# Kernel tuning notes

Hardware: AMD Instinct MI355X
Metric: run time of the kernel (lower is better)

## Reference

```python
import jax, jax.numpy as jnp
import numpy as np

N = 100000


def gcn_conv(x, W, b, src, dst, deg_inv_sqrt, n):
    # PyG GCNConv: h = D^{-1/2} (A + I) D^{-1/2} (x W) + b
    h = x @ W  # [N, out]
    norm = deg_inv_sqrt[src] * deg_inv_sqrt[dst]  # [E+N]
    msgs = h[src] * norm[:, None]  # gathered + scaled messages
    out = jax.ops.segment_sum(msgs, dst, num_segments=n)
    return out + b


def _self_loops_and_norm(edge_index, n):
    src, dst = edge_index[0], edge_index[1]
    loop = jnp.arange(n, dtype=edge_index.dtype)
    src = jnp.concatenate([src, loop])
    dst = jnp.concatenate([dst, loop])
    deg = jax.ops.segment_sum(jnp.ones_like(dst, dtype=jnp.float32), dst, num_segments=n)
    deg_inv_sqrt = jnp.where(deg > 0, jax.lax.rsqrt(jnp.maximum(deg, 1.0)), 0.0)
    return src, dst, deg_inv_sqrt


def setup_inputs() -> dict:
    key = jax.random.key(0)
    k1, k2, k3, k4 = jax.random.split(key, 4)
    nfeat, nhid, nclass = 512, 256, 40
    E = 3200000
    x = jax.random.normal(k1, (N, nfeat), dtype=jnp.float32)
    edge_index = jax.random.randint(k2, (2, E), 0, N, dtype=jnp.int64)
    # Glorot-style init for GCNConv weights, zero bias (PyG default)
    W1 = jax.random.normal(k3, (nfeat, nhid), dtype=jnp.float32) / np.sqrt(nfeat)
    b1 = jnp.zeros((nhid,), dtype=jnp.float32)
    W2 = jax.random.normal(k4, (nhid, nclass), dtype=jnp.float32) / np.sqrt(nhid)
    b2 = jnp.zeros((nclass,), dtype=jnp.float32)
    return {"x": x, "W1": W1, "b1": b1, "W2": W2, "b2": b2, "edge_index": edge_index}


def reference(x, W1, b1, W2, b2, edge_index):
    src, dst, dis = _self_loops_and_norm(edge_index, N)
    h = gcn_conv(x, W1, b1, src, dst, dis, N)
    h = jax.nn.relu(h)
    # dropout(p=0.5) is identity in eval mode
    h = gcn_conv(h, W2, b2, src, dst, dis, N)
    return jax.nn.log_softmax(h, axis=1)
```

## Files before the change

kernel.cpp:

```cpp
#include <hip/hip_runtime.h>
#include <math.h>

#define NFEAT 512
#define NHID  256
#define NCLASS 40
#define NBUCK 782
#define BCAP  5120

typedef __attribute__((ext_vector_type(8))) short short8;
typedef __attribute__((ext_vector_type(4))) float f32x4;


__device__ __forceinline__ float bflo(unsigned u) {
    union { unsigned i; float f; } x; x.i = u << 16; return x.f;
}
__device__ __forceinline__ float bfhi(unsigned u) {
    union { unsigned i; float f; } x; x.i = u & 0xffff0000u; return x.f;
}
__device__ __forceinline__ unsigned short f2bf(float f) {
    union { float f; unsigned i; } x; x.f = f;
    unsigned r = x.i + 0x7fffu + ((x.i >> 16) & 1u);
    return (unsigned short)(r >> 16);
}
__device__ __forceinline__ unsigned pack2(float a, float b) {
    return (unsigned)f2bf(a) | ((unsigned)f2bf(b) << 16);
}


__global__ __launch_bounds__(256) void partcast_k(const float* __restrict__ W1,
                                                  unsigned short* __restrict__ WT,
                                                  const int* __restrict__ ei,
                                                  int* bucketCnt,
                                                  unsigned* __restrict__ binned, int E) {
    __shared__ int hist[NBUCK];
    __shared__ int sbase[NBUCK];
    __shared__ int lofs[NBUCK];
    int bid = blockIdx.x;
    int t = threadIdx.x;
    if (bid < (NFEAT * NHID) / 256) {
        int idx = bid * 256 + t;
        int k = idx >> 8;
        int nn = idx & 255;
        WT[(size_t)nn * NFEAT + k] = f2bf(W1[idx]);
        return;
    }
    int pb = bid - (NFEAT * NHID) / 256;
    for (int b = t; b < NBUCK; b += 256) { hist[b] = 0; lofs[b] = 0; }
    __syncthreads();
    int chunk = (E + 255) / 256;
    int beg = pb * chunk;
    int end = beg + chunk; if (end > E) end = E;
    for (int e = beg + t; e < end; e += 256) {
        int d = __builtin_nontemporal_load(ei + (size_t)E + e);
        atomicAdd(&hist[d >> 7], 1);
    }
    __syncthreads();
    for (int b = t; b < NBUCK; b += 256) {
        int h = hist[b];
        if (h) sbase[b] = atomicAdd(&bucketCnt[b], h);
    }
    __syncthreads();
    for (int e = beg + t; e < end; e += 256) {
        int s = __builtin_nontemporal_load(ei + e);
        int d = __builtin_nontemporal_load(ei + (size_t)E + e);
        int b = d >> 7;
        int off = sbase[b] + atomicAdd(&lofs[b], 1);
        __builtin_nontemporal_store(((unsigned)s << 7) | (unsigned)(d & 127),
                                    binned + (size_t)b * BCAP + off);
    }
}


__global__ __launch_bounds__(1024) void bscan_k(const int* __restrict__ bucketCnt,
                                                int* __restrict__ bbase,
                                                int* __restrict__ offs, int n, int E) {
    __shared__ int sd[1024];
    int t = threadIdx.x;
    int v = (t < NBUCK) ? bucketCnt[t] : 0;
    sd[t] = v;
    __syncthreads();
    for (int off = 1; off < 1024; off <<= 1) {
        int add = (t >= off) ? sd[t - off] : 0;
        __syncthreads();
        sd[t] += add;
        __syncthreads();
    }
    if (t < NBUCK) bbase[t] = sd[t] - v;
    if (t == 0) offs[n] = E;
}


__global__ __launch_bounds__(512) void fill2_k(const unsigned* __restrict__ binned,
                                               const int* __restrict__ bucketCnt,
                                               const int* __restrict__ bbase,
                                               int* __restrict__ offs,
                                               float* __restrict__ dis,
                                               int* __restrict__ csrs, int n) {
    __shared__ int h128[128];
    __shared__ int sd[128];
    __shared__ int lcur[128];
    int b = blockIdx.x;
    int t = threadIdx.x;
    int node0 = b << 7;
    int cbt = bucketCnt[b];
    size_t base_in = (size_t)b * BCAP;
    int gbase = bbase[b];
    if (t < 128) h128[t] = 0;
    __syncthreads();
    for (int e = t; e < cbt; e += 512) {
        unsigned u = binned[base_in + e];
        atomicAdd(&h128[u & 127], 1);
    }
    __syncthreads();
    int v = (t < 128) ? h128[t] : 0;
    if (t < 128) sd[t] = v;
    __syncthreads();
    for (int off = 1; off < 128; off <<= 1) {
        int add = (t < 128 && t >= off) ? sd[t - off] : 0;
        __syncthreads();
        if (t < 128) sd[t] += add;
        __syncthreads();
    }
    if (t < 128) {
        int excl = sd[t] - v;
        int nd = node0 + t;
        if (nd < n) {
            offs[nd] = gbase + excl;
            dis[nd] = rsqrtf((float)v + 1.0f);
        }
        lcur[t] = gbase + excl;
    }
    __syncthreads();
    for (int e = t; e < cbt; e += 512) {
        unsigned u = binned[base_in + e];
        int pos = atomicAdd(&lcur[u & 127], 1);
        csrs[pos] = (int)(u >> 7);
    }
}


__global__ __launch_bounds__(256) void gemm1_k(const float* __restrict__ X,
                                               const unsigned short* __restrict__ WT,
                                               const float* __restrict__ dis,
                                               unsigned short* __restrict__ H, int M) {
    __shared__ unsigned short as[64][72];
    __shared__ unsigned short bs[256][72];
    int t = threadIdx.x;
    int lane = t & 63;
    int w = t >> 6;
    int m0 = blockIdx.x * 64;
    int quad = lane >> 4;
    int r16 = lane & 15;

    f32x4 acc[4][4];
#pragma unroll
    for (int a = 0; a < 4; ++a)
#pragma unroll
        for (int b = 0; b < 4; ++b) acc[a][b] = (f32x4){0.f, 0.f, 0.f, 0.f};

    for (int k0 = 0; k0 < NFEAT; k0 += 64) {
        {
            int m = t >> 2;
            int c = (t & 3) * 16;
            int gi = m0 + m;
            float4 v0, v1, v2, v3;
            if (gi < M) {
                const float4* p = (const float4*)(X + (size_t)gi * NFEAT + k0 + c);
                v0 = p[0]; v1 = p[1]; v2 = p[2]; v3 = p[3];
            } else {
                v0 = v1 = v2 = v3 = make_float4(0.f, 0.f, 0.f, 0.f);
            }
            uint4 p0, p1;
            p0.x = pack2(v0.x, v0.y); p0.y = pack2(v0.z, v0.w);
            p0.z = pack2(v1.x, v1.y); p0.w = pack2(v1.z, v1.w);
            p1.x = pack2(v2.x, v2.y); p1.y = pack2(v2.z, v2.w);
            p1.z = pack2(v3.x, v3.y); p1.w = pack2(v3.z, v3.w);
            *(uint4*)&as[m][c] = p0;
            *(uint4*)&as[m][c + 8] = p1;
        }
        {
            const uint4* p = (const uint4*)(WT + (size_t)t * NFEAT + k0);
#pragma unroll
            for (int c = 0; c < 8; ++c) {
                uint4 q = p[c];
                *(uint4*)&bs[t][c * 8] = q;
            }
        }
        __syncthreads();
#pragma unroll
        for (int ks = 0; ks < 64; ks += 32) {
            short8 af[4], bfr[4];
#pragma unroll
            for (int sm = 0; sm < 4; ++sm)
                af[sm] = *(const short8*)&as[sm * 16 + r16][ks + quad * 8];
#pragma unroll
            for (int sn = 0; sn < 4; ++sn)
                bfr[sn] = *(const short8*)&bs[w * 64 + sn * 16 + r16][ks + quad * 8];
#pragma unroll
            for (int sm = 0; sm < 4; ++sm)
#pragma unroll
                for (int sn = 0; sn < 4; ++sn)
                    acc[sm][sn] = __builtin_amdgcn_mfma_f32_16x16x32_bf16(
                        af[sm], bfr[sn], acc[sm][sn], 0, 0, 0);
        }
        __syncthreads();
    }
#pragma unroll
    for (int sm = 0; sm < 4; ++sm) {
#pragma unroll
        for (int rr = 0; rr < 4; ++rr) {
            int row = m0 + sm * 16 + quad * 4 + rr;
            if (row < M) {
                float dsc = dis[row];
#pragma unroll
                for (int sn = 0; sn < 4; ++sn) {
                    int col = w * 64 + sn * 16 + r16;
                    H[(size_t)row * NHID + col] = f2bf(acc[sm][sn][rr] * dsc);
                }
            }
        }
    }
}


__global__ __launch_bounds__(256) void agg1h_k(const unsigned short* __restrict__ Hb,
                                               const int* __restrict__ offs,
                                               const int* __restrict__ csrs,
                                               const float* __restrict__ dis,
                                               const float* __restrict__ b1,
                                               unsigned short* __restrict__ outb,
                                               int n, int f0u) {
    int lane = threadIdx.x & 63;
    int i = blockIdx.x * 4 + (threadIdx.x >> 6);
    if (i >= n) return;
    const unsigned* Hv = (const unsigned*)Hb;
    int col = f0u + lane;
    float a0 = 0.f, a1 = 0.f;
    int beg = offs[i], end = offs[i + 1];
    int e = beg;
    {
        int c[16]; unsigned g[16];
        for (; e + 16 <= end; e += 16) {
#pragma unroll
            for (int u = 0; u < 16; ++u) c[u] = csrs[e + u];
#pragma unroll
            for (int u = 0; u < 16; ++u) g[u] = Hv[(size_t)c[u] * 128 + col];
#pragma unroll
            for (int u = 0; u < 16; ++u) {
                a0 += bflo(g[u]); a1 += bfhi(g[u]);
            }
        }
        if (e < end) {
#pragma unroll
            for (int u = 0; u < 16; ++u)
                c[u] = (e + u < end) ? csrs[e + u] : i;
#pragma unroll
            for (int u = 0; u < 16; ++u) g[u] = Hv[(size_t)c[u] * 128 + col];
#pragma unroll
            for (int u = 0; u < 16; ++u) {
                float sel = (e + u < end) ? 1.f : 0.f;
                a0 = fmaf(sel, bflo(g[u]), a0); a1 = fmaf(sel, bfhi(g[u]), a1);
            }
        }
    }
    unsigned v = Hv[(size_t)i * 128 + col];
    a0 += bflo(v); a1 += bfhi(v);
    float di = dis[i];
    float2 bb = ((const float2*)b1)[col];
    a0 = fmaxf(fmaf(a0, di, bb.x), 0.f);
    a1 = fmaxf(fmaf(a1, di, bb.y), 0.f);
    ((unsigned*)outb)[(size_t)i * 128 + col] = pack2(a0, a1);
}


__global__ __launch_bounds__(256) void gemm2_k(const unsigned short* __restrict__ Ab,
                                               const float* __restrict__ W2,
                                               const float* __restrict__ dis,
                                               unsigned short* __restrict__ H2b, int M) {
    __shared__ float w2t[NCLASS][260];
    int t = threadIdx.x;
    for (int idx = t; idx < NHID * NCLASS; idx += 256) {
        int k = idx / NCLASS;
        int j = idx - k * NCLASS;
        w2t[j][k] = W2[idx];
    }
    __syncthreads();
    int i = blockIdx.x * 32 + (t >> 3);
    if (i >= M) return;
    int j0 = (t & 7) * 5;
    const uint2* arow = (const uint2*)(Ab + (size_t)i * NHID);
    float acc[5] = {0.f, 0.f, 0.f, 0.f, 0.f};
#pragma unroll 4
    for (int c = 0; c < 64; ++c) {
        uint2 v = arow[c];
        float a0 = bflo(v.x), a1 = bfhi(v.x), a2 = bflo(v.y), a3 = bfhi(v.y);
        int k = c * 4;
#pragma unroll
        for (int jj = 0; jj < 5; ++jj) {
            float4 q = *(const float4*)&w2t[j0 + jj][k];
            acc[jj] += a0 * q.x + a1 * q.y + a2 * q.z + a3 * q.w;
        }
    }
    float di = dis[i];
#pragma unroll
    for (int jj = 0; jj < 5; ++jj)
        H2b[(size_t)i * 64 + j0 + jj] = f2bf(acc[jj] * di);
    if ((t & 7) < 3)
        ((uint4*)(H2b + (size_t)i * 64 + 40))[t & 7] = make_uint4(0u, 0u, 0u, 0u);
}


__global__ __launch_bounds__(256) void agg2_k(const unsigned short* __restrict__ H2b,
                                              const int* __restrict__ offs,
                                              const int* __restrict__ csrs,
                                              const float* __restrict__ dis,
                                              const float* __restrict__ b2,
                                              float* __restrict__ out, int n) {
    int lane = threadIdx.x & 63;
    int i = blockIdx.x * 4 + (threadIdx.x >> 6);
    if (i >= n) return;
    const uint2* Hv = (const uint2*)H2b;
    int slot = lane >> 4;
    int r16 = lane & 15;
    float a0 = 0.f, a1 = 0.f, a2 = 0.f, a3 = 0.f;
    int beg = offs[i], end = offs[i + 1];
    int e = beg;
    {
        int c[8]; uint2 g[8];
        for (; e + 32 <= end; e += 32) {
#pragma unroll
            for (int u = 0; u < 8; ++u) c[u] = csrs[e + u * 4 + slot];
#pragma unroll
            for (int u = 0; u < 8; ++u) g[u] = Hv[(size_t)c[u] * 16 + r16];
#pragma unroll
            for (int u = 0; u < 8; ++u) {
                a0 += bflo(g[u].x); a1 += bfhi(g[u].x);
                a2 += bflo(g[u].y); a3 += bfhi(g[u].y);
            }
        }
        if (e < end) {
#pragma unroll
            for (int u = 0; u < 8; ++u) {
                int idx = e + u * 4 + slot;
                c[u] = (idx < end) ? csrs[idx] : i;
            }
#pragma unroll
            for (int u = 0; u < 8; ++u) g[u] = Hv[(size_t)c[u] * 16 + r16];
#pragma unroll
            for (int u = 0; u < 8; ++u) {
                float sel = (e + u * 4 + slot < end) ? 1.f : 0.f;
                a0 = fmaf(sel, bflo(g[u].x), a0); a1 = fmaf(sel, bfhi(g[u].x), a1);
                a2 = fmaf(sel, bflo(g[u].y), a2); a3 = fmaf(sel, bfhi(g[u].y), a3);
            }
        }
    }
    if (slot == 0) {
        uint2 v = Hv[(size_t)i * 16 + r16];
        a0 += bflo(v.x); a1 += bfhi(v.x);
        a2 += bflo(v.y); a3 += bfhi(v.y);
    }
    a0 += __shfl_xor(a0, 16, 64); a0 += __shfl_xor(a0, 32, 64);
    a1 += __shfl_xor(a1, 16, 64); a1 += __shfl_xor(a1, 32, 64);
    a2 += __shfl_xor(a2, 16, 64); a2 += __shfl_xor(a2, 32, 64);
    a3 += __shfl_xor(a3, 16, 64); a3 += __shfl_xor(a3, 32, 64);
    float di = dis[i];
    bool act = (r16 < 10);
    float4 bb = act ? ((const float4*)b2)[r16] : make_float4(0.f, 0.f, 0.f, 0.f);
    a0 = fmaf(a0, di, bb.x); a1 = fmaf(a1, di, bb.y);
    a2 = fmaf(a2, di, bb.z); a3 = fmaf(a3, di, bb.w);
    float m = act ? fmaxf(fmaxf(a0, a1), fmaxf(a2, a3)) : -INFINITY;
#pragma unroll
    for (int off = 8; off > 0; off >>= 1) m = fmaxf(m, __shfl_xor(m, off, 16));
    float s = act ? (expf(a0 - m) + expf(a1 - m) + expf(a2 - m) + expf(a3 - m)) : 0.f;
#pragma unroll
    for (int off = 8; off > 0; off >>= 1) s += __shfl_xor(s, off, 16);
    float ls = m + logf(s);
    if (lane < 10) {
        float4 o = make_float4(a0 - ls, a1 - ls, a2 - ls, a3 - ls);
        ((float4*)(out + (size_t)i * NCLASS))[lane] = o;
    }
}


extern "C" void kernel_launch(void* const* d_in, const int* in_sizes, int n_in,
                              void* d_out, int out_size, void* d_ws, size_t ws_size,
                              hipStream_t stream) {
    const float* x  = (const float*)d_in[0];
    const float* W1 = (const float*)d_in[1];
    const float* b1 = (const float*)d_in[2];
    const float* W2 = (const float*)d_in[3];
    const float* b2 = (const float*)d_in[4];
    const int*   ei = (const int*)d_in[5];

    const int N = in_sizes[0] / NFEAT;
    const int E = in_sizes[5] / 2;

    size_t off = 0;
    auto alloc = [&](size_t bytes) { size_t o = off; off += (bytes + 255) & ~(size_t)255; return o; };
    char* ws = (char*)d_ws;
    int*            offs    = (int*)           (ws + alloc((size_t)(N + 1) * 4));
    float*          dis     = (float*)         (ws + alloc((size_t)N * 4));
    int*            bcnt    = (int*)           (ws + alloc((size_t)NBUCK * 4));
    int*            bbase   = (int*)           (ws + alloc((size_t)NBUCK * 4));
    unsigned*       binned  = (unsigned*)      (ws + alloc((size_t)NBUCK * BCAP * 4));
    int*            csrs    = (int*)           (ws + alloc((size_t)E * 4));
    unsigned short* wT      = (unsigned short*)(ws + alloc((size_t)NFEAT * NHID * 2));
    unsigned short* h1b     = (unsigned short*)(ws + alloc((size_t)N * NHID * 2));
    unsigned short* a1b     = (unsigned short*)(ws + alloc((size_t)N * NHID * 2));
    unsigned short* h2b     = (unsigned short*)(ws + alloc((size_t)N * 64 * 2));
    float*          out     = (float*)d_out;

    hipMemsetAsync(bcnt, 0, (size_t)NBUCK * 4, stream);
    partcast_k<<<(NFEAT * NHID) / 256 + 256, 256, 0, stream>>>(W1, wT, ei, bcnt, binned, E);
    bscan_k<<<1, 1024, 0, stream>>>(bcnt, bbase, offs, N, E);
    fill2_k<<<NBUCK, 512, 0, stream>>>(binned, bcnt, bbase, offs, dis, csrs, N);
    gemm1_k<<<(N + 63) / 64, 256, 0, stream>>>(x, wT, dis, h1b, N);
    agg1h_k<<<(N + 3) / 4, 256, 0, stream>>>(h1b, offs, csrs, dis, b1, a1b, N, 0);
    agg1h_k<<<(N + 3) / 4, 256, 0, stream>>>(h1b, offs, csrs, dis, b1, a1b, N, 64);
    gemm2_k<<<(N + 31) / 32, 256, 0, stream>>>(a1b, W2, dis, h2b, N);
    agg2_k<<<(N + 3) / 4, 256, 0, stream>>>(h2b, offs, csrs, dis, b2, out, N);
}
```

Measured before the change: 801.4 us.

## Stage binned edges in LDS and write buckets contiguously in partition kernel

The edge-partition kernel now sorts each chunk's packed edges by bucket in shared memory, using a block-wide prefix scan of the histogram. It then writes each bucket's run to global memory with one wavefront per bucket, so stores are contiguous instead of scattered. The chunk size is fixed at 8192 edges, which raises the block count from 256 to about 391 for better occupancy and parallelism. In exchange it adds an in-block scan, about 32KB of LDS per block, and extra barriers, and it drops the nontemporal load and store hints.

```diff
diff --git a/kernel.cpp b/kernel.cpp
--- a/kernel.cpp
+++ b/kernel.cpp
@@ -6,6 +6,7 @@
 #define NCLASS 40
 #define NBUCK 782
 #define BCAP  5120
+#define PCHUNK 8192
 
 typedef __attribute__((ext_vector_type(8))) short short8;
 typedef __attribute__((ext_vector_type(4))) float f32x4;
@@ -32,9 +33,12 @@
                                                   const int* __restrict__ ei,
                                                   int* bucketCnt,
                                                   unsigned* __restrict__ binned, int E) {
+    __shared__ unsigned staged[PCHUNK];
     __shared__ int hist[NBUCK];
+    __shared__ int lofs[NBUCK];
     __shared__ int sbase[NBUCK];
-    __shared__ int lofs[NBUCK];
+    __shared__ int lcur[NBUCK];
+    __shared__ int wsum[256];
     int bid = blockIdx.x;
     int t = threadIdx.x;
     if (bid < (NFEAT * NHID) / 256) {
@@ -45,28 +49,60 @@
         return;
     }
     int pb = bid - (NFEAT * NHID) / 256;
-    for (int b = t; b < NBUCK; b += 256) { hist[b] = 0; lofs[b] = 0; }
-    __syncthreads();
-    int chunk = (E + 255) / 256;
-    int beg = pb * chunk;
-    int end = beg + chunk; if (end > E) end = E;
+    int beg = pb * PCHUNK;
+    int end = beg + PCHUNK; if (end > E) end = E;
+
+    for (int b = t; b < NBUCK; b += 256) hist[b] = 0;
+    __syncthreads();
     for (int e = beg + t; e < end; e += 256) {
-        int d = __builtin_nontemporal_load(ei + (size_t)E + e);
+        int d = ei[(size_t)E + e];
         atomicAdd(&hist[d >> 7], 1);
+    }
+    __syncthreads();
+    int v[4];
+    int s0 = 0;
+#pragma unroll
+    for (int r = 0; r < 4; ++r) {
+        int idx = t * 4 + r;
+        v[r] = (idx < NBUCK) ? hist[idx] : 0;
+        s0 += v[r];
+    }
+    wsum[t] = s0;
+    __syncthreads();
+    for (int off = 1; off < 256; off <<= 1) {
+        int add = (t >= off) ? wsum[t - off] : 0;
+        __syncthreads();
+        wsum[t] += add;
+        __syncthreads();
+    }
+    int excl = wsum[t] - s0;
+#pragma unroll
+    for (int r = 0; r < 4; ++r) {
+        int idx = t * 4 + r;
+        if (idx < NBUCK) { lofs[idx] = excl; lcur[idx] = excl; }
+        excl += v[r];
     }
     __syncthreads();
     for (int b = t; b < NBUCK; b += 256) {
         int h = hist[b];
         if (h) sbase[b] = atomicAdd(&bucketCnt[b], h);
     }
-    __syncthreads();
     for (int e = beg + t; e < end; e += 256) {
-        int s = __builtin_nontemporal_load(ei + e);
-        int d = __builtin_nontemporal_load(ei + (size_t)E + e);
+        int s = ei[e];
+        int d = ei[(size_t)E + e];
         int b = d >> 7;
-        int off = sbase[b] + atomicAdd(&lofs[b], 1);
-        __builtin_nontemporal_store(((unsigned)s << 7) | (unsigned)(d & 127),
-                                    binned + (size_t)b * BCAP + off);
+        int p = atomicAdd(&lcur[b], 1);
+        staged[p] = ((unsigned)s << 7) | (unsigned)(d & 127);
+    }
+    __syncthreads();
+    int w = t >> 6, lane = t & 63;
+    for (int b = w; b < NBUCK; b += 4) {
+        int h = hist[b];
+        if (!h) continue;
+        int lo = lofs[b];
+        size_t gb = (size_t)b * BCAP + sbase[b];
+        for (int l = lane; l < h; l += 64)
+            binned[gb + l] = staged[lo + l];
     }
 }
 
@@ -410,8 +446,10 @@
     unsigned short* h2b     = (unsigned short*)(ws + alloc((size_t)N * 64 * 2));
     float*          out     = (float*)d_out;
 
+    int npart = (E + PCHUNK - 1) / PCHUNK;
+
     hipMemsetAsync(bcnt, 0, (size_t)NBUCK * 4, stream);
-    partcast_k<<<(NFEAT * NHID) / 256 + 256, 256, 0, stream>>>(W1, wT, ei, bcnt, binned, E);
+    partcast_k<<<(NFEAT * NHID) / 256 + npart, 256, 0, stream>>>(W1, wT, ei, bcnt, binned, E);
     bscan_k<<<1, 1024, 0, stream>>>(bcnt, bbase, offs, N, E);
     fill2_k<<<NBUCK, 512, 0, stream>>>(binned, bcnt, bbase, offs, dis, csrs, N);
     gemm1_k<<<(N + 63) / 64, 256, 0, stream>>>(x, wT, dis, h1b, N);
```

New measurement: 768.4 us. -4.1%, faster.
